# Kernel optimization log

Measured on AMD Instinct MI355X. Metric: run time of the kernel, lower is better.

Reference implementation:

```python
import jax, jax.numpy as jnp
import numpy as np

H = 16           # attn_num
ROPE_THETA = 10000.0

def _rope(x):
    # x: [B, H, S, A]; non-interleaved (rotate-half) RoPE matching RotaryEmb
    A = x.shape[-1]
    S = x.shape[2]
    inv_freq = (1.0 / ROPE_THETA) ** (jnp.arange(0, A, 2, dtype=jnp.float32) / A)  # [A/2]
    t = jnp.arange(S, dtype=jnp.float32)
    freqs = t[:, None] * inv_freq[None, :]            # [S, A/2]
    cos = jnp.cos(freqs)[None, None, :, :]
    sin = jnp.sin(freqs)[None, None, :, :]
    x1, x2 = jnp.split(x, 2, axis=-1)
    y1 = x1 * cos + x2 * sin
    y2 = -x1 * sin + x2 * cos
    return jnp.concatenate([y1, y2], axis=-1).astype(x.dtype)

def setup_inputs() -> dict:
    key = jax.random.key(0)
    kq, kk, kv = jax.random.split(key, 3)
    B, S, D = 2, 2048, 2048
    return {
        "xq": jax.random.normal(kq, (B, S, D), dtype=jnp.float32),
        "xk": jax.random.normal(kk, (B, S, D), dtype=jnp.float32),
        "xv": jax.random.normal(kv, (B, S, D), dtype=jnp.float32),
    }

def reference(xq, xk, xv):
    B, S, D = xq.shape
    A = D // H
    # b s (h a) -> b h s a
    q = xq.reshape(B, S, H, A).transpose(0, 2, 1, 3)
    k = xk.reshape(B, S, H, A).transpose(0, 2, 1, 3)
    v = xv.reshape(B, S, H, A).transpose(0, 2, 1, 3)
    q = _rope(q)
    k = _rope(k)
    scale = 1.0 / jnp.sqrt(jnp.asarray(A, dtype=q.dtype))
    scores = jnp.einsum('bhsa,bhta->bhst', q, k) * scale   # [B,H,S,S]
    causal = jnp.tril(jnp.ones((S, S), dtype=bool))
    scores = jnp.where(causal[None, None, :, :], scores, jnp.asarray(-jnp.inf, scores.dtype))
    probs = jax.nn.softmax(scores, axis=-1)
    out = jnp.einsum('bhst,bhta->bhsa', probs, v)          # [B,H,S,A]
    # b h s a -> b s (h a)
    return out.transpose(0, 2, 1, 3).reshape(B, S, D)
```

## Files before the change

kernel.cpp:

```cpp
#include <hip/hip_runtime.h>
#include <stdint.h>

#define H_HEADS 16
#define ADIM    128
#define SLEN    2048
#define DMODEL  2048

typedef __attribute__((ext_vector_type(8))) short  short8;
typedef __attribute__((ext_vector_type(4))) float  float4v;
typedef __attribute__((ext_vector_type(4))) unsigned short ushort4v;

typedef const __attribute__((address_space(1))) unsigned int gas_u32;
typedef __attribute__((address_space(3))) unsigned int las_u32;

union F4 { float4 v; float a[4]; };
union PU { unsigned u[4]; short8 s; };

struct CTrue  { static constexpr bool value = true;  };
struct CFalse { static constexpr bool value = false; };

__device__ __forceinline__ unsigned short f2bf(float f) {
  union { float f; unsigned u; } v; v.f = f;
  unsigned r = v.u + 0x7FFFu + ((v.u >> 16) & 1u);
  return (unsigned short)(r >> 16);
}

__device__ __forceinline__ unsigned cvt_pk_bf16(float lo, float hi) {
  unsigned r;
  asm("v_cvt_pk_bf16_f32 %0, %1, %2" : "=v"(r) : "v"(lo), "v"(hi));
  return r;
}

__device__ __forceinline__ void xswap(unsigned& a, unsigned& b) {
  asm volatile("v_permlane32_swap_b32 %0, %1" : "+v"(a), "+v"(b));
  asm volatile("v_permlane16_swap_b32 %0, %1" : "+v"(a), "+v"(b));
}

#define ROPE_C 0.20762050593045935f
#define C2LOG  0.12751879523103988f
#define THRZ   11.0f

__global__ __launch_bounds__(256) void prep_k(const float* __restrict__ xk,
                                              unsigned short* __restrict__ kw) {
  int t = blockIdx.x * 256 + threadIdx.x;
  int i4 = t & 15;
  int h  = (t >> 4) & (H_HEADS - 1);
  int s  = (t >> 8) & (SLEN - 1);
  int b  = t >> 19;
  int i0 = i4 * 4;
  long ib = ((long)(b * SLEN + s)) * DMODEL + h * ADIM;
  F4 x1, x2;
  x1.v = *(const float4*)(xk + ib + i0);
  x2.v = *(const float4*)(xk + ib + i0 + 64);
  ushort4v o1, o2;
  #pragma unroll
  for (int j = 0; j < 4; ++j) {
    float inv = exp2f(-(float)(i0 + j) * ROPE_C);
    float ang = (float)s * inv;
    float sn, cs;
    sincosf(ang, &sn, &cs);
    o1[j] = f2bf( x1.a[j] * cs + x2.a[j] * sn);
    o2[j] = f2bf(-x1.a[j] * sn + x2.a[j] * cs);
  }
  long row = ((long)((b * H_HEADS + h) * SLEN + s)) * ADIM;
  int swz = s & 7;
  int c1 = ((((i0     ) >> 3) ^ swz) << 3) | (i0 & 7);
  int c2 = ((((i0 + 64) >> 3) ^ swz) << 3) | (i0 & 7);
  *(ushort4v*)(kw + row + c1) = o1;
  *(ushort4v*)(kw + row + c2) = o2;
}

__global__ __launch_bounds__(256) void prep_v(const float* __restrict__ xv,
                                              unsigned short* __restrict__ vw) {
  __shared__ float lv[64 * 129];
  int jt = blockIdx.x;
  int bh = blockIdx.y;
  int b = bh >> 4, h = bh & (H_HEADS - 1);
  int t = threadIdx.x;
  #pragma unroll
  for (int it = 0; it < 8; ++it) {
    int id  = it * 256 + t;
    int row = id >> 5;
    int c4  = (id & 31) * 4;
    F4 x;
    x.v = *(const float4*)(xv + ((long)(b * SLEN + jt * 64 + row)) * DMODEL + h * ADIM + c4);
    #pragma unroll
    for (int j = 0; j < 4; ++j) lv[row * 129 + c4 + j] = x.a[j];
  }
  __syncthreads();
  int l = t & 63, w = t >> 6;
  unsigned short* vt = vw + ((long)(bh * 32 + jt)) * 8192;
  #pragma unroll
  for (int it = 0; it < 8; ++it) {
    int d = it * 16 + w * 4 + (l >> 4);
    int i = l & 15;
    ushort4v o;
    #pragma unroll
    for (int j = 0; j < 4; ++j) o[j] = f2bf(lv[(4 * i + j) * 129 + d]);
    int off = d * 64 + ((((i >> 1) ^ (d & 7)) << 3) | ((i & 1) << 2));
    *(ushort4v*)(vt + off) = o;
  }
}

__global__ __launch_bounds__(256, 2) void attn_fwd(const float* __restrict__ xq,
                                                   const unsigned short* __restrict__ kw,
                                                   const unsigned short* __restrict__ vw,
                                                   float* __restrict__ out) {
  __shared__ __align__(16) unsigned short kL[2][64 * 128];
  __shared__ __align__(16) unsigned short vL[2][128 * 64];

  int bh = blockIdx.x;
  int pi = blockIdx.y;
  int qtA = 31 - pi, qtB = pi;
  int b = bh >> 4, h = bh & (H_HEADS - 1);
  int t = threadIdx.x, l = t & 63, w = t >> 6;
  int lq = l & 15, g = l >> 4, lq7 = lq & 7;

  int sqA = qtA * 64 + w * 16 + lq;
  int sqB = qtB * 64 + w * 16 + lq;

  short8 qfA[4], qfB[4];
  auto ROPEQ = [&](int sq, short8 (&qf)[4]) {
    const float* qsrc = xq + ((long)(b * SLEN + sq)) * DMODEL + h * ADIM;
    float q32[4][8];
    #pragma unroll
    for (int c = 0; c < 4; ++c) {
      F4 lo, hi;
      lo.v = *(const float4*)(qsrc + c * 32 + g * 8);
      hi.v = *(const float4*)(qsrc + c * 32 + g * 8 + 4);
      #pragma unroll
      for (int j = 0; j < 4; ++j) { q32[c][j] = lo.a[j]; q32[c][j + 4] = hi.a[j]; }
    }
    #pragma unroll
    for (int c = 0; c < 2; ++c) {
      #pragma unroll
      for (int j = 0; j < 8; ++j) {
        int a = c * 32 + g * 8 + j;
        float inv = exp2f(-(float)a * ROPE_C);
        float ang = (float)sq * inv;
        float sn, cs;
        sincosf(ang, &sn, &cs);
        qf[c    ][j] = (short)f2bf( q32[c][j] * cs + q32[c + 2][j] * sn);
        qf[c + 2][j] = (short)f2bf(-q32[c][j] * sn + q32[c + 2][j] * cs);
      }
    }
  };
  ROPEQ(sqA, qfA);
  ROPEQ(sqB, qfB);

  float4v accA[8], accB[8];
  #pragma unroll
  for (int i = 0; i < 8; ++i) { accA[i] = (float4v){0.f,0.f,0.f,0.f}; accB[i] = (float4v){0.f,0.f,0.f,0.f}; }
  float mA = -1e30f, lA = 0.f, mB = -1e30f, lB = 0.f;

  const unsigned short* kbase_g = kw + (long)bh * SLEN * ADIM;
  const unsigned short* vbase_g = vw + (long)bh * 32 * 8192;

  auto STAGE = [&](int bufi, int jn) {
    const unsigned short* ks = kbase_g + (long)jn * (64 * ADIM);
    const unsigned short* vs = vbase_g + (long)jn * 8192;
    #pragma unroll
    for (int sg = 0; sg < 4; ++sg) {
      int seg = w * 4 + sg;
      __builtin_amdgcn_global_load_lds((gas_u32*)(ks + seg * 512 + l * 8),
                                       (las_u32*)&kL[bufi][seg * 512], 16, 0, 0);
      __builtin_amdgcn_global_load_lds((gas_u32*)(vs + seg * 512 + l * 8),
                                       (las_u32*)&vL[bufi][seg * 512], 16, 0, 0);
    }
  };

  auto SOFTMAX = [&](float4v (&sv)[4], float& m_z, float& l_run, float4v (&acc)[8],
                     int sq, int qt, int jt, short8 (&pa)[2]) {
    float s[16];
    #pragma unroll
    for (int kb = 0; kb < 4; ++kb)
      #pragma unroll
      for (int r = 0; r < 4; ++r) s[kb * 4 + r] = sv[kb][r];
    if (jt == qt) {
      #pragma unroll
      for (int kb = 0; kb < 4; ++kb)
        #pragma unroll
        for (int r = 0; r < 4; ++r)
          if (qt * 64 + kb * 16 + g * 4 + r > sq) s[kb * 4 + r] = -1e30f;
    }
    float t0 = fmaxf(fmaxf(s[0], s[1]),   fmaxf(s[2], s[3]));
    float t1 = fmaxf(fmaxf(s[4], s[5]),   fmaxf(s[6], s[7]));
    float t2 = fmaxf(fmaxf(s[8], s[9]),   fmaxf(s[10], s[11]));
    float t3 = fmaxf(fmaxf(s[12], s[13]), fmaxf(s[14], s[15]));
    float tm = fmaxf(fmaxf(t0, t1), fmaxf(t2, t3));
    tm = fmaxf(tm, __shfl_xor(tm, 16));
    tm = fmaxf(tm, __shfl_xor(tm, 32));
    float zt = tm * C2LOG;
    if (!__all(zt <= m_z + THRZ)) {
      float mn = fmaxf(m_z, zt);
      float corr = exp2f(m_z - mn);
      m_z = mn;
      l_run *= corr;
      float cb[4];
      #pragma unroll
      for (int r = 0; r < 4; ++r) cb[r] = __shfl(corr, g * 4 + r);
      #pragma unroll
      for (int db = 0; db < 8; ++db)
        #pragma unroll
        for (int r = 0; r < 4; ++r) acc[db][r] *= cb[r];
    }
    float p[16];
    float ts = 0.f;
    #pragma unroll
    for (int i = 0; i < 16; ++i) { p[i] = exp2f(fmaf(s[i], C2LOG, -m_z)); ts += p[i]; }
    l_run += ts;

    unsigned L[4], Hh[4];
    #pragma unroll
    for (int kb = 0; kb < 4; ++kb) {
      L[kb]  = cvt_pk_bf16(p[kb * 4 + 0], p[kb * 4 + 1]);
      Hh[kb] = cvt_pk_bf16(p[kb * 4 + 2], p[kb * 4 + 3]);
    }
    xswap(L[0], L[1]);  xswap(Hh[0], Hh[1]);
    xswap(L[2], L[3]);  xswap(Hh[2], Hh[3]);
    PU a0, a1;
    a0.u[0] = L[0]; a0.u[1] = Hh[0]; a0.u[2] = L[1]; a0.u[3] = Hh[1];
    a1.u[0] = L[2]; a1.u[1] = Hh[2]; a1.u[2] = L[3]; a1.u[3] = Hh[3];
    pa[0] = a0.s; pa[1] = a1.s;
  };

  auto QK = [&](auto BOTH, int cur, float4v (&sA)[4], float4v (&sB)[4]) {
    const unsigned short* kl = &kL[cur][0];
    __builtin_amdgcn_s_setprio(1);
    #pragma unroll
    for (int c = 0; c < 4; ++c) {
      int koff = ((c * 4 + g) ^ lq7) << 3;
      #pragma unroll
      for (int kb = 0; kb < 4; ++kb) {
        short8 kf = *(const short8*)&kl[(kb * 16 + lq) * 128 + koff];
        sA[kb] = __builtin_amdgcn_mfma_f32_16x16x32_bf16(kf, qfA[c], sA[kb], 0, 0, 0);
        if constexpr (decltype(BOTH)::value)
          sB[kb] = __builtin_amdgcn_mfma_f32_16x16x32_bf16(kf, qfB[c], sB[kb], 0, 0, 0);
      }
    }
    __builtin_amdgcn_s_setprio(0);
  };

  auto PV = [&](auto BOTH, int cur, short8 (&paA)[2], short8 (&paB)[2]) {
    const unsigned short* vl = &vL[cur][0];
    __builtin_amdgcn_s_setprio(1);
    #pragma unroll
    for (int kc = 0; kc < 2; ++kc) {
      int ch = ((kc * 4 + g) ^ lq7) << 3;
      #pragma unroll
      for (int db = 0; db < 8; ++db) {
        short8 vb = *(const short8*)&vl[(db * 16 + lq) * 64 + ch];
        accA[db] = __builtin_amdgcn_mfma_f32_16x16x32_bf16(paA[kc], vb, accA[db], 0, 0, 0);
        if constexpr (decltype(BOTH)::value)
          accB[db] = __builtin_amdgcn_mfma_f32_16x16x32_bf16(paB[kc], vb, accB[db], 0, 0, 0);
      }
    }
    __builtin_amdgcn_s_setprio(0);
  };

  STAGE(0, 0);
  asm volatile("s_waitcnt vmcnt(0)" ::: "memory");
  __builtin_amdgcn_s_barrier();
  int cur = 0;

  for (int jt = 0; jt <= qtA; ++jt) {
    if (jt < qtA) STAGE(cur ^ 1, jt + 1);
    bool doB = (jt <= qtB);
    float4v sA[4], sB[4];
    #pragma unroll
    for (int i = 0; i < 4; ++i) { sA[i] = (float4v){0.f,0.f,0.f,0.f}; sB[i] = (float4v){0.f,0.f,0.f,0.f}; }
    short8 paA[2], paB[2];
    if (doB) QK(CTrue{},  cur, sA, sB);
    else     QK(CFalse{}, cur, sA, sB);
    SOFTMAX(sA, mA, lA, accA, sqA, qtA, jt, paA);
    if (doB) SOFTMAX(sB, mB, lB, accB, sqB, qtB, jt, paB);
    if (doB) PV(CTrue{},  cur, paA, paB);
    else     PV(CFalse{}, cur, paA, paB);
    asm volatile("s_waitcnt vmcnt(0)" ::: "memory");
    __builtin_amdgcn_s_barrier();
    cur ^= 1;
  }

  auto EPI = [&](int qt, float l_run, float4v (&acc)[8]) {
    float lt = l_run + __shfl_xor(l_run, 16);
    lt += __shfl_xor(lt, 32);
    float linv = 1.0f / lt;
    float lb[4];
    #pragma unroll
    for (int r = 0; r < 4; ++r) lb[r] = __shfl(linv, g * 4 + r);
    #pragma unroll
    for (int db = 0; db < 8; ++db)
      #pragma unroll
      for (int r = 0; r < 4; ++r)
        out[((long)(b * SLEN + qt * 64 + w * 16 + g * 4 + r)) * DMODEL + h * ADIM + db * 16 + lq]
          = acc[db][r] * lb[r];
  };
  EPI(qtA, lA, accA);
  EPI(qtB, lB, accB);
}

extern "C" void kernel_launch(void* const* d_in, const int* in_sizes, int n_in,
                              void* d_out, int out_size, void* d_ws, size_t ws_size,
                              hipStream_t stream) {
  const float* xq = (const float*)d_in[0];
  const float* xk = (const float*)d_in[1];
  const float* xv = (const float*)d_in[2];
  float* outp = (float*)d_out;
  int B = in_sizes[0] / (SLEN * DMODEL);
  size_t perT = (size_t)B * H_HEADS * SLEN * ADIM;
  unsigned short* kw = (unsigned short*)d_ws;
  unsigned short* vw = kw + perT;

  prep_k<<<dim3(B * 2048), 256, 0, stream>>>(xk, kw);
  prep_v<<<dim3(32, B * H_HEADS), 256, 0, stream>>>(xv, vw);
  attn_fwd<<<dim3(B * H_HEADS, 16), 256, 0, stream>>>(xq, kw, vw, outp);
}
```

Before: 88.12 us.

## Split paired q-tiles into one tile per block with 32-key tiles and fast RoPE

```diff
diff --git a/kernel.cpp b/kernel.cpp
--- a/kernel.cpp
+++ b/kernel.cpp
@@ -16,9 +16,6 @@
 union F4 { float4 v; float a[4]; };
 union PU { unsigned u[4]; short8 s; };
 
-struct CTrue  { static constexpr bool value = true;  };
-struct CFalse { static constexpr bool value = false; };
-
 __device__ __forceinline__ unsigned short f2bf(float f) {
   union { float f; unsigned u; } v; v.f = f;
   unsigned r = v.u + 0x7FFFu + ((v.u >> 16) & 1u);
@@ -36,7 +33,12 @@
   asm volatile("v_permlane16_swap_b32 %0, %1" : "+v"(a), "+v"(b));
 }
 
+__device__ __forceinline__ float fsin01(float r) { float o; asm("v_sin_f32 %0, %1" : "=v"(o) : "v"(r)); return o; }
+__device__ __forceinline__ float fcos01(float r) { float o; asm("v_cos_f32 %0, %1" : "=v"(o) : "v"(r)); return o; }
+__device__ __forceinline__ float ffract(float x) { float o; asm("v_fract_f32 %0, %1" : "=v"(o) : "v"(x)); return o; }
+
 #define ROPE_C 0.20762050593045935f
+#define L2I2PI -2.651496129472319f
 #define C2LOG  0.12751879523103988f
 #define THRZ   11.0f
 
@@ -55,10 +57,9 @@
   ushort4v o1, o2;
   #pragma unroll
   for (int j = 0; j < 4; ++j) {
-    float inv = exp2f(-(float)(i0 + j) * ROPE_C);
-    float ang = (float)s * inv;
-    float sn, cs;
-    sincosf(ang, &sn, &cs);
+    float rev = (float)s * exp2f(fmaf(-(float)(i0 + j), ROPE_C, L2I2PI));
+    float r = ffract(rev);
+    float sn = fsin01(r), cs = fcos01(r);
     o1[j] = f2bf( x1.a[j] * cs + x2.a[j] * sn);
     o2[j] = f2bf(-x1.a[j] * sn + x2.a[j] * cs);
   }
@@ -72,96 +73,89 @@
 
 __global__ __launch_bounds__(256) void prep_v(const float* __restrict__ xv,
                                               unsigned short* __restrict__ vw) {
-  __shared__ float lv[64 * 129];
+  __shared__ float lv[32 * 129];
   int jt = blockIdx.x;
   int bh = blockIdx.y;
   int b = bh >> 4, h = bh & (H_HEADS - 1);
   int t = threadIdx.x;
   #pragma unroll
-  for (int it = 0; it < 8; ++it) {
+  for (int it = 0; it < 4; ++it) {
     int id  = it * 256 + t;
     int row = id >> 5;
     int c4  = (id & 31) * 4;
     F4 x;
-    x.v = *(const float4*)(xv + ((long)(b * SLEN + jt * 64 + row)) * DMODEL + h * ADIM + c4);
+    x.v = *(const float4*)(xv + ((long)(b * SLEN + jt * 32 + row)) * DMODEL + h * ADIM + c4);
     #pragma unroll
     for (int j = 0; j < 4; ++j) lv[row * 129 + c4 + j] = x.a[j];
   }
   __syncthreads();
-  int l = t & 63, w = t >> 6;
-  unsigned short* vt = vw + ((long)(bh * 32 + jt)) * 8192;
-  #pragma unroll
-  for (int it = 0; it < 8; ++it) {
-    int d = it * 16 + w * 4 + (l >> 4);
-    int i = l & 15;
+  unsigned short* vt = vw + ((long)(bh * 64 + jt)) * 4096;
+  #pragma unroll
+  for (int it = 0; it < 4; ++it) {
+    int id = it * 256 + t;
+    int d  = id >> 3;
+    int i  = id & 7;
     ushort4v o;
     #pragma unroll
     for (int j = 0; j < 4; ++j) o[j] = f2bf(lv[(4 * i + j) * 129 + d]);
-    int off = d * 64 + ((((i >> 1) ^ (d & 7)) << 3) | ((i & 1) << 2));
+    int off = d * 32 + ((((i >> 1) ^ (d & 3)) << 3) | ((i & 1) << 2));
     *(ushort4v*)(vt + off) = o;
   }
 }
 
-__global__ __launch_bounds__(256, 2) void attn_fwd(const float* __restrict__ xq,
+__global__ __launch_bounds__(256, 4) void attn_fwd(const float* __restrict__ xq,
                                                    const unsigned short* __restrict__ kw,
                                                    const unsigned short* __restrict__ vw,
                                                    float* __restrict__ out) {
-  __shared__ __align__(16) unsigned short kL[2][64 * 128];
-  __shared__ __align__(16) unsigned short vL[2][128 * 64];
-
-  int bh = blockIdx.x;
-  int pi = blockIdx.y;
-  int qtA = 31 - pi, qtB = pi;
+  __shared__ __align__(16) unsigned short kL[2][32 * 128];
+  __shared__ __align__(16) unsigned short vL[2][128 * 32];
+
+  int n  = blockIdx.x;
+  int qt = 31 - (n >> 5);
+  int bh = n & 31;
   int b = bh >> 4, h = bh & (H_HEADS - 1);
   int t = threadIdx.x, l = t & 63, w = t >> 6;
-  int lq = l & 15, g = l >> 4, lq7 = lq & 7;
-
-  int sqA = qtA * 64 + w * 16 + lq;
-  int sqB = qtB * 64 + w * 16 + lq;
-
-  short8 qfA[4], qfB[4];
-  auto ROPEQ = [&](int sq, short8 (&qf)[4]) {
-    const float* qsrc = xq + ((long)(b * SLEN + sq)) * DMODEL + h * ADIM;
-    float q32[4][8];
-    #pragma unroll
-    for (int c = 0; c < 4; ++c) {
-      F4 lo, hi;
-      lo.v = *(const float4*)(qsrc + c * 32 + g * 8);
-      hi.v = *(const float4*)(qsrc + c * 32 + g * 8 + 4);
-      #pragma unroll
-      for (int j = 0; j < 4; ++j) { q32[c][j] = lo.a[j]; q32[c][j + 4] = hi.a[j]; }
-    }
-    #pragma unroll
-    for (int c = 0; c < 2; ++c) {
-      #pragma unroll
-      for (int j = 0; j < 8; ++j) {
-        int a = c * 32 + g * 8 + j;
-        float inv = exp2f(-(float)a * ROPE_C);
-        float ang = (float)sq * inv;
-        float sn, cs;
-        sincosf(ang, &sn, &cs);
-        qf[c    ][j] = (short)f2bf( q32[c][j] * cs + q32[c + 2][j] * sn);
-        qf[c + 2][j] = (short)f2bf(-q32[c][j] * sn + q32[c + 2][j] * cs);
-      }
-    }
-  };
-  ROPEQ(sqA, qfA);
-  ROPEQ(sqB, qfB);
-
-  float4v accA[8], accB[8];
-  #pragma unroll
-  for (int i = 0; i < 8; ++i) { accA[i] = (float4v){0.f,0.f,0.f,0.f}; accB[i] = (float4v){0.f,0.f,0.f,0.f}; }
-  float mA = -1e30f, lA = 0.f, mB = -1e30f, lB = 0.f;
+  int lq = l & 15, g = l >> 4, lq7 = lq & 7, lq3 = lq & 3;
+  int sq = qt * 64 + w * 16 + lq;
+
+  const float* qsrc = xq + ((long)(b * SLEN + sq)) * DMODEL + h * ADIM;
+  float q32[4][8];
+  #pragma unroll
+  for (int c = 0; c < 4; ++c) {
+    F4 lo, hi;
+    lo.v = *(const float4*)(qsrc + c * 32 + g * 8);
+    hi.v = *(const float4*)(qsrc + c * 32 + g * 8 + 4);
+    #pragma unroll
+    for (int j = 0; j < 4; ++j) { q32[c][j] = lo.a[j]; q32[c][j + 4] = hi.a[j]; }
+  }
+  short8 qf[4];
+  #pragma unroll
+  for (int c = 0; c < 2; ++c) {
+    #pragma unroll
+    for (int j = 0; j < 8; ++j) {
+      int a = c * 32 + g * 8 + j;
+      float rev = (float)sq * exp2f(fmaf(-(float)a, ROPE_C, L2I2PI));
+      float r = ffract(rev);
+      float sn = fsin01(r), cs = fcos01(r);
+      qf[c    ][j] = (short)f2bf( q32[c][j] * cs + q32[c + 2][j] * sn);
+      qf[c + 2][j] = (short)f2bf(-q32[c][j] * sn + q32[c + 2][j] * cs);
+    }
+  }
+
+  float4v acc[8];
+  #pragma unroll
+  for (int i = 0; i < 8; ++i) acc[i] = (float4v){0.f, 0.f, 0.f, 0.f};
+  float m_z = -1e30f, l_run = 0.f;
 
   const unsigned short* kbase_g = kw + (long)bh * SLEN * ADIM;
-  const unsigned short* vbase_g = vw + (long)bh * 32 * 8192;
+  const unsigned short* vbase_g = vw + (long)bh * 64 * 4096;
 
   auto STAGE = [&](int bufi, int jn) {
-    const unsigned short* ks = kbase_g + (long)jn * (64 * ADIM);
-    const unsigned short* vs = vbase_g + (long)jn * 8192;
-    #pragma unroll
-    for (int sg = 0; sg < 4; ++sg) {
-      int seg = w * 4 + sg;
+    const unsigned short* ks = kbase_g + (long)jn * (32 * ADIM);
+    const unsigned short* vs = vbase_g + (long)jn * 4096;
+    #pragma unroll
+    for (int i = 0; i < 2; ++i) {
+      int seg = w * 2 + i;
       __builtin_amdgcn_global_load_lds((gas_u32*)(ks + seg * 512 + l * 8),
                                        (las_u32*)&kL[bufi][seg * 512], 16, 0, 0);
       __builtin_amdgcn_global_load_lds((gas_u32*)(vs + seg * 512 + l * 8),
@@ -169,25 +163,47 @@
     }
   };
 
-  auto SOFTMAX = [&](float4v (&sv)[4], float& m_z, float& l_run, float4v (&acc)[8],
-                     int sq, int qt, int jt, short8 (&pa)[2]) {
-    float s[16];
-    #pragma unroll
-    for (int kb = 0; kb < 4; ++kb)
+  int nt = 2 * qt + 2;
+
+  STAGE(0, 0);
+  asm volatile("s_waitcnt vmcnt(0)" ::: "memory");
+  __builtin_amdgcn_s_barrier();
+  int cur = 0;
+
+  for (int jt = 0; jt < nt; ++jt) {
+    if (jt < nt - 1) STAGE(cur ^ 1, jt + 1);
+
+    float4v sv[2];
+    sv[0] = (float4v){0.f, 0.f, 0.f, 0.f};
+    sv[1] = (float4v){0.f, 0.f, 0.f, 0.f};
+    const unsigned short* kl = &kL[cur][0];
+    __builtin_amdgcn_s_setprio(1);
+    #pragma unroll
+    for (int c = 0; c < 4; ++c) {
+      int koff = ((c * 4 + g) ^ lq7) << 3;
+      #pragma unroll
+      for (int kb = 0; kb < 2; ++kb) {
+        short8 kf = *(const short8*)&kl[(kb * 16 + lq) * 128 + koff];
+        sv[kb] = __builtin_amdgcn_mfma_f32_16x16x32_bf16(kf, qf[c], sv[kb], 0, 0, 0);
+      }
+    }
+    __builtin_amdgcn_s_setprio(0);
+
+    float s[8];
+    #pragma unroll
+    for (int kb = 0; kb < 2; ++kb)
       #pragma unroll
       for (int r = 0; r < 4; ++r) s[kb * 4 + r] = sv[kb][r];
-    if (jt == qt) {
-      #pragma unroll
-      for (int kb = 0; kb < 4; ++kb)
+    if (jt >= 2 * qt) {
+      #pragma unroll
+      for (int kb = 0; kb < 2; ++kb)
         #pragma unroll
         for (int r = 0; r < 4; ++r)
-          if (qt * 64 + kb * 16 + g * 4 + r > sq) s[kb * 4 + r] = -1e30f;
-    }
-    float t0 = fmaxf(fmaxf(s[0], s[1]),   fmaxf(s[2], s[3]));
-    float t1 = fmaxf(fmaxf(s[4], s[5]),   fmaxf(s[6], s[7]));
-    float t2 = fmaxf(fmaxf(s[8], s[9]),   fmaxf(s[10], s[11]));
-    float t3 = fmaxf(fmaxf(s[12], s[13]), fmaxf(s[14], s[15]));
-    float tm = fmaxf(fmaxf(t0, t1), fmaxf(t2, t3));
+          if (jt * 32 + kb * 16 + g * 4 + r > sq) s[kb * 4 + r] = -1e30f;
+    }
+    float t0 = fmaxf(fmaxf(s[0], s[1]), fmaxf(s[2], s[3]));
+    float t1 = fmaxf(fmaxf(s[4], s[5]), fmaxf(s[6], s[7]));
+    float tm = fmaxf(t0, t1);
     tm = fmaxf(tm, __shfl_xor(tm, 16));
     tm = fmaxf(tm, __shfl_xor(tm, 32));
     float zt = tm * C2LOG;
@@ -204,99 +220,48 @@
         #pragma unroll
         for (int r = 0; r < 4; ++r) acc[db][r] *= cb[r];
     }
-    float p[16];
+    float p[8];
     float ts = 0.f;
     #pragma unroll
-    for (int i = 0; i < 16; ++i) { p[i] = exp2f(fmaf(s[i], C2LOG, -m_z)); ts += p[i]; }
+    for (int i = 0; i < 8; ++i) { p[i] = exp2f(fmaf(s[i], C2LOG, -m_z)); ts += p[i]; }
     l_run += ts;
 
-    unsigned L[4], Hh[4];
-    #pragma unroll
-    for (int kb = 0; kb < 4; ++kb) {
-      L[kb]  = cvt_pk_bf16(p[kb * 4 + 0], p[kb * 4 + 1]);
-      Hh[kb] = cvt_pk_bf16(p[kb * 4 + 2], p[kb * 4 + 3]);
-    }
-    xswap(L[0], L[1]);  xswap(Hh[0], Hh[1]);
-    xswap(L[2], L[3]);  xswap(Hh[2], Hh[3]);
-    PU a0, a1;
-    a0.u[0] = L[0]; a0.u[1] = Hh[0]; a0.u[2] = L[1]; a0.u[3] = Hh[1];
-    a1.u[0] = L[2]; a1.u[1] = Hh[2]; a1.u[2] = L[3]; a1.u[3] = Hh[3];
-    pa[0] = a0.s; pa[1] = a1.s;
-  };
-
-  auto QK = [&](auto BOTH, int cur, float4v (&sA)[4], float4v (&sB)[4]) {
-    const unsigned short* kl = &kL[cur][0];
-    __builtin_amdgcn_s_setprio(1);
-    #pragma unroll
-    for (int c = 0; c < 4; ++c) {
-      int koff = ((c * 4 + g) ^ lq7) << 3;
-      #pragma unroll
-      for (int kb = 0; kb < 4; ++kb) {
-        short8 kf = *(const short8*)&kl[(kb * 16 + lq) * 128 + koff];
-        sA[kb] = __builtin_amdgcn_mfma_f32_16x16x32_bf16(kf, qfA[c], sA[kb], 0, 0, 0);
-        if constexpr (decltype(BOTH)::value)
-          sB[kb] = __builtin_amdgcn_mfma_f32_16x16x32_bf16(kf, qfB[c], sB[kb], 0, 0, 0);
-      }
-    }
-    __builtin_amdgcn_s_setprio(0);
-  };
-
-  auto PV = [&](auto BOTH, int cur, short8 (&paA)[2], short8 (&paB)[2]) {
+    unsigned L0 = cvt_pk_bf16(p[0], p[1]);
+    unsigned H0 = cvt_pk_bf16(p[2], p[3]);
+    unsigned L1 = cvt_pk_bf16(p[4], p[5]);
+    unsigned H1 = cvt_pk_bf16(p[6], p[7]);
+    xswap(L0, L1);
+    xswap(H0, H1);
+    PU pa;
+    pa.u[0] = L0; pa.u[1] = H0; pa.u[2] = L1; pa.u[3] = H1;
+
     const unsigned short* vl = &vL[cur][0];
     __builtin_amdgcn_s_setprio(1);
     #pragma unroll
-    for (int kc = 0; kc < 2; ++kc) {
-      int ch = ((kc * 4 + g) ^ lq7) << 3;
-      #pragma unroll
-      for (int db = 0; db < 8; ++db) {
-        short8 vb = *(const short8*)&vl[(db * 16 + lq) * 64 + ch];
-        accA[db] = __builtin_amdgcn_mfma_f32_16x16x32_bf16(paA[kc], vb, accA[db], 0, 0, 0);
-        if constexpr (decltype(BOTH)::value)
-          accB[db] = __builtin_amdgcn_mfma_f32_16x16x32_bf16(paB[kc], vb, accB[db], 0, 0, 0);
-      }
+    for (int db = 0; db < 8; ++db) {
+      int ch = (g ^ lq3) << 3;
+      short8 vb = *(const short8*)&vl[(db * 16 + lq) * 32 + ch];
+      acc[db] = __builtin_amdgcn_mfma_f32_16x16x32_bf16(pa.s, vb, acc[db], 0, 0, 0);
     }
     __builtin_amdgcn_s_setprio(0);
-  };
-
-  STAGE(0, 0);
-  asm volatile("s_waitcnt vmcnt(0)" ::: "memory");
-  __builtin_amdgcn_s_barrier();
-  int cur = 0;
-
-  for (int jt = 0; jt <= qtA; ++jt) {
-    if (jt < qtA) STAGE(cur ^ 1, jt + 1);
-    bool doB = (jt <= qtB);
-    float4v sA[4], sB[4];
-    #pragma unroll
-    for (int i = 0; i < 4; ++i) { sA[i] = (float4v){0.f,0.f,0.f,0.f}; sB[i] = (float4v){0.f,0.f,0.f,0.f}; }
-    short8 paA[2], paB[2];
-    if (doB) QK(CTrue{},  cur, sA, sB);
-    else     QK(CFalse{}, cur, sA, sB);
-    SOFTMAX(sA, mA, lA, accA, sqA, qtA, jt, paA);
-    if (doB) SOFTMAX(sB, mB, lB, accB, sqB, qtB, jt, paB);
-    if (doB) PV(CTrue{},  cur, paA, paB);
-    else     PV(CFalse{}, cur, paA, paB);
+
     asm volatile("s_waitcnt vmcnt(0)" ::: "memory");
     __builtin_amdgcn_s_barrier();
     cur ^= 1;
   }
 
-  auto EPI = [&](int qt, float l_run, float4v (&acc)[8]) {
-    float lt = l_run + __shfl_xor(l_run, 16);
-    lt += __shfl_xor(lt, 32);
-    float linv = 1.0f / lt;
-    float lb[4];
-    #pragma unroll
-    for (int r = 0; r < 4; ++r) lb[r] = __shfl(linv, g * 4 + r);
-    #pragma unroll
-    for (int db = 0; db < 8; ++db)
-      #pragma unroll
-      for (int r = 0; r < 4; ++r)
-        out[((long)(b * SLEN + qt * 64 + w * 16 + g * 4 + r)) * DMODEL + h * ADIM + db * 16 + lq]
-          = acc[db][r] * lb[r];
-  };
-  EPI(qtA, lA, accA);
-  EPI(qtB, lB, accB);
+  float lt = l_run + __shfl_xor(l_run, 16);
+  lt += __shfl_xor(lt, 32);
+  float linv = 1.0f / lt;
+  float lb[4];
+  #pragma unroll
+  for (int r = 0; r < 4; ++r) lb[r] = __shfl(linv, g * 4 + r);
+  #pragma unroll
+  for (int db = 0; db < 8; ++db)
+    #pragma unroll
+    for (int r = 0; r < 4; ++r)
+      out[((long)(b * SLEN + qt * 64 + w * 16 + g * 4 + r)) * DMODEL + h * ADIM + db * 16 + lq]
+        = acc[db][r] * lb[r];
 }
 
 extern "C" void kernel_launch(void* const* d_in, const int* in_sizes, int n_in,
@@ -312,6 +277,6 @@
   unsigned short* vw = kw + perT;
 
   prep_k<<<dim3(B * 2048), 256, 0, stream>>>(xk, kw);
-  prep_v<<<dim3(32, B * H_HEADS), 256, 0, stream>>>(xv, vw);
-  attn_fwd<<<dim3(B * H_HEADS, 16), 256, 0, stream>>>(xq, kw, vw, outp);
-}
+  prep_v<<<dim3(64, B * H_HEADS), 256, 0, stream>>>(xv, vw);
+  attn_fwd<<<dim3(B * H_HEADS * 32), 256, 0, stream>>>(xq, kw, vw, outp);
+}
```

New measurement: 96.89 us. 1.1x slower.
